# Optimization experiments

Hardware: AMD Instinct MI355X
Metric: run time of the kernel (lower is better)

The kernel has to match this reference:

```python
import jax, jax.numpy as jnp
import numpy as np

B, A, N_OBS, HX, N_ACT = 8192, 32, 128, 64, 16

def setup_inputs() -> dict:
    key = jax.random.key(0)
    ks = jax.random.split(key, 12)
    s = lambda *shape: 0.05 * jax.random.normal(ks[setup_inputs.i], shape, dtype=jnp.float32)
    out = {}
    setup_inputs.i = 0
    def nxt(*shape):
        setup_inputs.i += 1
        return 0.05 * jax.random.normal(ks[setup_inputs.i], shape, dtype=jnp.float32)
    out['obs'] = jax.random.normal(ks[0], (B, A, N_OBS), dtype=jnp.float32)
    out['W1'] = nxt(A, N_OBS, 128); out['b1'] = nxt(A, 128)
    out['W2'] = nxt(A, 128, HX);   out['b2'] = nxt(A, HX)
    out['Wg'] = nxt(A, HX, 2);     out['bg'] = nxt(A, 2)
    out['Wc'] = nxt(A, 2 * HX, HX); out['bc'] = nxt(A, HX)
    out['Wd'] = nxt(A, HX, N_ACT); out['bd'] = nxt(A, N_ACT)
    out['comm_mask'] = jax.random.randint(jax.random.fold_in(key, 99), (A, A), 0, 2, dtype=jnp.int32)
    return out

def reference(obs, W1, b1, W2, b2, Wg, bg, Wc, bc, Wd, bd, comm_mask):
    # encode: per-agent 2-layer MLP, batched over agents via einsum
    x = jax.nn.relu(jnp.einsum('ban,anh->bah', obs, W1) + b1)      # [B,A,128]
    h = jax.nn.relu(jnp.einsum('bah,ahk->bak', x, W2) + b2)        # [B,A,HX]
    # gate: Linear->ReLU->Softmax (computed as in original; only used via the
    # host-side RNG in the torch code, externalized here as comm_mask)
    gates = jax.nn.softmax(jax.nn.relu(jnp.einsum('bak,akg->bag', h, Wg) + bg), axis=-1)
    # communication: for agent i, mean of hidden states of communicating j != i
    mask = comm_mask.astype(h.dtype) * (1.0 - jnp.eye(A, dtype=h.dtype))  # [A_i, A_j]
    total = jnp.einsum('ij,bjk->bik', mask, h)                      # [B,A,HX]
    count = mask.sum(axis=1)                                        # [A]
    comm = total / jnp.maximum(count, 1.0)[None, :, None]           # count==0 -> zeros
    comm_in = jnp.concatenate([h, comm], axis=-1)                   # [B,A,2*HX]
    h2 = jnp.tanh(jnp.einsum('bac,ack->bak', comm_in, Wc) + bc)     # [B,A,HX]
    q = jnp.einsum('bak,akn->ban', h2, Wd) + bd                     # [B,A,N_ACT]
    return q
```

## Files before the change

kernel.cpp:

```cpp
#include <hip/hip_runtime.h>


#define NB   8192
#define NA   32
#define NOBS 128
#define NH1  128
#define HXX  64
#define NACT 16

typedef _Float16 half8 __attribute__((ext_vector_type(8)));
typedef _Float16 half4 __attribute__((ext_vector_type(4)));
typedef float    floatx4 __attribute__((ext_vector_type(4)));

#define MFMA16(af, bf, c) __builtin_amdgcn_mfma_f32_16x16x32_f16((af), (bf), (c), 0, 0, 0)
#define H8(x) __builtin_bit_cast(half8, (x))

#define HWS_OFF 0
#define W1P_OFF (NB * NA * HXX)
#define W1P_CNT (NA * 8 * 4 * 512)
#define W2P_OFF (W1P_OFF + W1P_CNT)
#define W2P_CNT (NA * 4 * 4 * 512)
#define WCP_OFF (W2P_OFF + W2P_CNT)
#define WCP_CNT (NA * 4 * 4 * 512)
#define WDP_OFF (WCP_OFF + WCP_CNT)
#define WDP_CNT (NA * 1 * 2 * 512)
#define MN_OFF  (WDP_OFF + WDP_CNT)

#define HSTR 2056
#define DEC_LDS (16 * HSTR * 2)

#define ENC_TILES 16
#define ENC_WROWS 256
#define ENC_BROWS 1024
#define ENC_DEPTH 4
#define ENC_SLAB  (ENC_DEPTH * 8192)
#define ENC_W2LDS (4 * ENC_SLAB)
#define ENC_LDS   (ENC_W2LDS + 16384)

#define PK_FRAG_BLOCKS 528
#define PK_BLOCKS      (PK_FRAG_BLOCKS + 4)

using gas1p = const __attribute__((address_space(1))) void*;
using las3p = __attribute__((address_space(3))) void*;

__device__ __forceinline__ float fast_tanh(float x) {
    x = fminf(fmaxf(x, -10.f), 10.f);
    float e2 = __expf(2.f * x);
    return (e2 - 1.f) / (e2 + 1.f);
}

extern "C" __global__ __launch_bounds__(256)
void pack_kernel(const float* __restrict__ W1,
                 const float* __restrict__ W2,
                 const float* __restrict__ Wc,
                 const float* __restrict__ Wd,
                 const int*   __restrict__ cmask,
                 _Float16* __restrict__ ws)
{
    __shared__ float stg[4][512];
    const int bid = blockIdx.x, tid = threadIdx.x;

    if (bid >= PK_FRAG_BLOCKS) {
        int r = (bid - PK_FRAG_BLOCKS) * 256 + tid;
        if (r >= NA * NA) return;
        int i = r >> 5, j = r & 31;
        int c = 0;
        for (int jj = 0; jj < NA; ++jj) c += (jj != i && cmask[i * NA + jj]) ? 1 : 0;
        float v = 0.f;
        if (j != i && cmask[i * NA + j]) v = 1.0f / (float)(c > 1 ? c : 1);
        ((float*)(ws + MN_OFF))[r] = v;
        return;
    }

    const int w = tid >> 6, l = tid & 63;
    const int W = bid * 4 + w;

    const float* src; _Float16* dst; int K, N;
    int a, nt, s;
    if (W < 1024) {
        int q = W; a = q >> 5; nt = (q >> 2) & 7; s = q & 3;
        src = W1; N = 128; K = 128;
        dst = ws + W1P_OFF + ((a * 8 + nt) * 4 + s) * 512;
    } else if (W < 1536) {
        int q = W - 1024; a = q >> 4; nt = (q >> 2) & 3; s = q & 3;
        src = W2; N = 64; K = 128;
        dst = ws + W2P_OFF + ((a * 4 + nt) * 4 + s) * 512;
    } else if (W < 2048) {
        int q = W - 1536; a = q >> 4; nt = (q >> 2) & 3; s = q & 3;
        src = Wc; N = 64; K = 128;
        dst = ws + WCP_OFF + ((a * 4 + nt) * 4 + s) * 512;
    } else {
        int q = W - 2048; a = q >> 1; nt = 0; s = q & 1;
        src = Wd; N = 16; K = 64;
        dst = ws + WDP_OFF + (a * 2 + s) * 512;
    }

    const float* base = src + (size_t)a * K * N + (size_t)(s * 32) * N + nt * 16;
    float* S = stg[w];

    #pragma unroll
    for (int p = 0; p < 8; ++p) {
        int e = p * 64 + l, kk = e >> 4, nn = e & 15;
        S[kk * 16 + nn] = base[(size_t)kk * N + nn];
    }
    asm volatile("s_waitcnt lgkmcnt(0)" ::: "memory");
    __builtin_amdgcn_sched_barrier(0);

    half8 hv;
    #pragma unroll
    for (int j = 0; j < 8; ++j)
        hv[j] = (_Float16)S[((l >> 4) * 8 + j) * 16 + (l & 15)];
    *(half8*)&dst[l * 8] = hv;
}

__device__ __forceinline__ void enc_wait_vm(int t) {
    switch (t) {
    case 0:  asm volatile("s_waitcnt vmcnt(24)" ::: "memory"); break;
    case 1:  asm volatile("s_waitcnt vmcnt(26)" ::: "memory"); break;
    case 2:  asm volatile("s_waitcnt vmcnt(28)" ::: "memory"); break;
    case 13: asm volatile("s_waitcnt vmcnt(22)" ::: "memory"); break;
    case 14: asm volatile("s_waitcnt vmcnt(14)" ::: "memory"); break;
    case 15: asm volatile("s_waitcnt vmcnt(6)"  ::: "memory"); break;
    default: asm volatile("s_waitcnt vmcnt(30)" ::: "memory"); break;
    }
}

extern "C" __global__ __launch_bounds__(256, 1)
void enc_kernel(const float* __restrict__ obs,
                const float* __restrict__ b1,
                const float* __restrict__ b2,
                const _Float16* __restrict__ W1p,
                const _Float16* __restrict__ W2p,
                _Float16* __restrict__ hws)
{
    extern __shared__ char smem[];

    const int tid  = threadIdx.x;
    const int a    = blockIdx.y;
    const int w    = tid >> 6, l = tid & 63;
    const int lm   = l & 15, lq = l >> 4;
    const int hrow = l >> 5;
    const int cch  = l & 31;
    char* SB = smem + w * ENC_SLAB;
    _Float16* W2L = (_Float16*)(smem + ENC_W2LDS);

    {
        const uint4* s = (const uint4*)(W2p + (size_t)a * (4 * 4 * 512));
        uint4* d = (uint4*)W2L;
        #pragma unroll
        for (int q = 0; q < 4; ++q) d[tid + 256 * q] = s[tid + 256 * q];
    }

    const int rowb = blockIdx.x * ENC_BROWS + w * ENC_WROWS;
    const char* ob = (const char*)obs + (size_t)rowb * (NA * NOBS * 4) + (size_t)a * (NOBS * 4);

    floatx4 w1r[8][4];
    #pragma unroll
    for (int nt = 0; nt < 8; ++nt)
        #pragma unroll
        for (int s = 0; s < 4; ++s)
            w1r[nt][s] = *(const floatx4*)&W1p[(((a * 8 + nt) * 4 + s) * 512) + l * 8];
    float b1v[8], b2v[4];
    #pragma unroll
    for (int nt = 0; nt < 8; ++nt) b1v[nt] = b1[a * NH1 + nt * 16 + lm];
    #pragma unroll
    for (int nt = 0; nt < 4; ++nt) b2v[nt] = b2[a * HXX + nt * 16 + lm];

    #pragma unroll
    for (int nt = 0; nt < 8; ++nt)
        #pragma unroll
        for (int s = 0; s < 4; ++s) asm volatile("" :: "v"(w1r[nt][s]));
    #pragma unroll
    for (int nt = 0; nt < 8; ++nt) asm volatile("" :: "v"(b1v[nt]));
    #pragma unroll
    for (int nt = 0; nt < 4; ++nt) asm volatile("" :: "v"(b2v[nt]));

    int dmaoff[8];
    #pragma unroll
    for (int i = 0; i < 8; ++i) {
        const int r = 2 * i + hrow;
        dmaoff[i] = r * (NA * NOBS * 4) + ((cch ^ (r & 7)) << 4);
    }

    auto issue = [&](int t) {
        const char* bt = ob + (size_t)t * (16 * NA * NOBS * 4);
        char* dstb = SB + (t & 3) * 8192;
        #pragma unroll
        for (int i = 0; i < 8; ++i)
            __builtin_amdgcn_global_load_lds((gas1p)(bt + dmaoff[i]),
                                             (las3p)(dstb + i * 1024), 16, 0, 0);
    };

    __syncthreads();

    issue(0); issue(1); issue(2);

    for (int t = 0; t < ENC_TILES; ++t) {
        char* SBp = SB + (t & 3) * 8192;

        asm volatile("s_waitcnt lgkmcnt(0)" ::: "memory");
        if (t <= ENC_TILES - 4) issue(t + 3);
        enc_wait_vm(t);
        __builtin_amdgcn_sched_barrier(0);

        _Float16* X = (_Float16*)SBp;
        const int rx = lm & 7;

        floatx4 acc1[8];
        #pragma unroll
        for (int nt = 0; nt < 8; ++nt) acc1[nt] = (floatx4){0.f, 0.f, 0.f, 0.f};
        #pragma unroll
        for (int s = 0; s < 4; ++s) {
            const int c0 = s * 8 + lq * 2;
            floatx4 f0 = *(const floatx4*)(SBp + lm * 512 + (((c0    ) ^ rx) << 4));
            floatx4 f1 = *(const floatx4*)(SBp + lm * 512 + (((c0 + 1) ^ rx) << 4));
            half8 af;
            af[0] = (_Float16)f0[0]; af[1] = (_Float16)f0[1];
            af[2] = (_Float16)f0[2]; af[3] = (_Float16)f0[3];
            af[4] = (_Float16)f1[0]; af[5] = (_Float16)f1[1];
            af[6] = (_Float16)f1[2]; af[7] = (_Float16)f1[3];
            #pragma unroll
            for (int nt = 0; nt < 8; ++nt)
                acc1[nt] = MFMA16(af, H8(w1r[nt][s]), acc1[nt]);
        }
        #pragma unroll
        for (int nt = 0; nt < 8; ++nt)
            #pragma unroll
            for (int v = 0; v < 4; ++v) {
                float xv = fmaxf(acc1[nt][v] + b1v[nt], 0.f);
                X[(lq * 4 + v) * 136 + nt * 16 + lm] = (_Float16)xv;
            }

        floatx4 acc2[4];
        #pragma unroll
        for (int nt = 0; nt < 4; ++nt) acc2[nt] = (floatx4){0.f, 0.f, 0.f, 0.f};
        #pragma unroll
        for (int s = 0; s < 4; ++s) {
            half8 af2 = *(const half8*)&X[lm * 136 + s * 32 + lq * 8];
            #pragma unroll
            for (int nt = 0; nt < 4; ++nt) {
                half8 bf = *(const half8*)&W2L[(nt * 4 + s) * 512 + l * 8];
                acc2[nt] = MFMA16(af2, bf, acc2[nt]);
            }
        }
        #pragma unroll
        for (int nt = 0; nt < 4; ++nt)
            #pragma unroll
            for (int v = 0; v < 4; ++v) {
                float hv = fmaxf(acc2[nt][v] + b2v[nt], 0.f);
                X[(lq * 4 + v) * 136 + nt * 16 + lm] = (_Float16)hv;
            }

        {
            const int rr = l >> 2, cc = l & 3;
            _Float16* hb = hws + ((size_t)(rowb + t * 16 + rr) * NA + a) * HXX;
            #pragma unroll
            for (int q2 = 0; q2 < 2; ++q2) {
                const int chunk = cc + 4 * q2;
                half8 hv8 = *(const half8*)&X[rr * 136 + chunk * 8];
                *(half8*)&hb[chunk * 8] = hv8;
            }
        }
    }
}

extern "C" __global__ __launch_bounds__(512)
void dec_kernel(const _Float16* __restrict__ hws,
                const float* __restrict__ MnG,
                const float* __restrict__ bc,
                const float* __restrict__ bd,
                const _Float16* __restrict__ Wcp,
                const _Float16* __restrict__ Wdp,
                float* __restrict__ out)
{
    extern __shared__ char smem[];
    _Float16* H = (_Float16*)smem;

    const int t  = threadIdx.x;
    const int b0 = blockIdx.x * 16;

    {
        const uint4* src = (const uint4*)(hws + (size_t)b0 * NA * HXX);
        #pragma unroll
        for (int it = 0; it < 8; ++it) {
            int idx = it * 512 + t;
            int row = idx >> 8, rem = idx & 255;
            *(uint4*)&H[row * HSTR + rem * 8] = src[idx];
        }
    }
    __syncthreads();

    const int w = t >> 6, l = t & 63, lm = l & 15, lq = l >> 4;

    half8 hacc[4][2];
    #pragma unroll
    for (int g = 0; g < 4; ++g)
        #pragma unroll
        for (int sb = 0; sb < 2; ++sb)
            #pragma unroll
            for (int q = 0; q < 8; ++q) hacc[g][sb][q] = (_Float16)0.f;

    #pragma unroll 4
    for (int j = 0; j < NA; ++j) {
        half8 v0 = *(const half8*)&H[lm * HSTR + j * 64 + lq * 8];
        half8 v1 = *(const half8*)&H[lm * HSTR + j * 64 + 32 + lq * 8];
        #pragma unroll
        for (int g = 0; g < 4; ++g) {
            int ag = __builtin_amdgcn_readfirstlane(w * 4 + g);
            _Float16 mh = (_Float16)MnG[ag * NA + j];
            hacc[g][0] += v0 * mh;
            hacc[g][1] += v1 * mh;
        }
    }
    __syncthreads();

    half4 h2r[4][4];
    #pragma unroll
    for (int nt = 0; nt < 4; ++nt) {
        floatx4 acc[4];
        #pragma unroll
        for (int g = 0; g < 4; ++g) acc[g] = (floatx4){0.f, 0.f, 0.f, 0.f};
        #pragma unroll
        for (int s = 0; s < 4; ++s) {
            #pragma unroll
            for (int g = 0; g < 4; ++g) {
                int ag = w * 4 + g;
                half8 af = (s < 2)
                    ? *(const half8*)&H[lm * HSTR + ag * 64 + s * 32 + lq * 8]
                    : hacc[g][s - 2];
                half8 bf = *(const half8*)&Wcp[(((ag * 4 + nt) * 4 + s) * 512) + l * 8];
                acc[g] = MFMA16(af, bf, acc[g]);
            }
        }
        #pragma unroll
        for (int g = 0; g < 4; ++g) {
            int ag = w * 4 + g;
            float bcv = bc[ag * HXX + nt * 16 + lm];
            #pragma unroll
            for (int v = 0; v < 4; ++v)
                h2r[g][nt][v] = (_Float16)fast_tanh(acc[g][v] + bcv);
        }
    }

    #pragma unroll
    for (int g = 0; g < 4; ++g) {
        int ag = w * 4 + g;
        #pragma unroll
        for (int nt = 0; nt < 4; ++nt)
            #pragma unroll
            for (int v = 0; v < 4; ++v)
                H[(lq * 4 + v) * HSTR + ag * 64 + nt * 16 + lm] = h2r[g][nt][v];
    }

    floatx4 acc3[4];
    #pragma unroll
    for (int g = 0; g < 4; ++g) acc3[g] = (floatx4){0.f, 0.f, 0.f, 0.f};
    #pragma unroll
    for (int s = 0; s < 2; ++s) {
        #pragma unroll
        for (int g = 0; g < 4; ++g) {
            int ag = w * 4 + g;
            half8 af = *(const half8*)&H[lm * HSTR + ag * 64 + s * 32 + lq * 8];
            half8 bf = *(const half8*)&Wdp[((ag * 2 + s) * 512) + l * 8];
            acc3[g] = MFMA16(af, bf, acc3[g]);
        }
    }

    #pragma unroll
    for (int g = 0; g < 4; ++g) {
        int ag = w * 4 + g;
        float bdv = bd[ag * NACT + lm];
        #pragma unroll
        for (int v = 0; v < 4; ++v) {
            int row = lq * 4 + v;
            out[((size_t)(b0 + row) * NA + ag) * NACT + lm] = acc3[g][v] + bdv;
        }
    }
}

extern "C" void kernel_launch(void* const* d_in, const int* in_sizes, int n_in,
                              void* d_out, int out_size, void* d_ws, size_t ws_size,
                              hipStream_t stream)
{
    const float* obs = (const float*)d_in[0];
    const float* W1  = (const float*)d_in[1];
    const float* b1  = (const float*)d_in[2];
    const float* W2  = (const float*)d_in[3];
    const float* b2  = (const float*)d_in[4];
    const float* Wc  = (const float*)d_in[7];
    const float* bc  = (const float*)d_in[8];
    const float* Wd  = (const float*)d_in[9];
    const float* bd  = (const float*)d_in[10];
    const int*   cm  = (const int*)d_in[11];

    float*    outp = (float*)d_out;
    _Float16* ws   = (_Float16*)d_ws;

    _Float16* hws = ws + HWS_OFF;
    _Float16* W1p = ws + W1P_OFF;
    _Float16* W2p = ws + W2P_OFF;
    _Float16* Wcp = ws + WCP_OFF;
    _Float16* Wdp = ws + WDP_OFF;
    const float* MnG = (const float*)(ws + MN_OFF);

    hipLaunchKernelGGL(pack_kernel, dim3(PK_BLOCKS), dim3(256), 0, stream,
                       W1, W2, Wc, Wd, cm, ws);

    (void)hipFuncSetAttribute((const void*)enc_kernel,
                              hipFuncAttributeMaxDynamicSharedMemorySize, ENC_LDS);
    hipLaunchKernelGGL(enc_kernel, dim3(NB / ENC_BROWS, NA), dim3(256), ENC_LDS,
                       stream, obs, b1, b2, W1p, W2p, hws);

    (void)hipFuncSetAttribute((const void*)dec_kernel,
                              hipFuncAttributeMaxDynamicSharedMemorySize, DEC_LDS);
    hipLaunchKernelGGL(dec_kernel, dim3(NB / 16), dim3(512), DEC_LDS, stream,
                       hws, MnG, bc, bd, Wcp, Wdp, outp);
}
```

Baseline: 275.5 us.

## Fuse encoder MLP into decoder kernel, dropping the hidden-state workspace round trip

Merges the per-agent encoder (two MFMA layers) into the decoder kernel, so each 512-thread block encodes its 16 batch rows for all 32 agents and writes h directly into LDS. This removes the fp16 h write to and reread from global memory, plus one launch. In exchange, the obs loads are plain global loads with no DMA pipelining, and W1/W2 fragments are reread from global/L2 by every block, where before they were kept in registers across 16 tiles.

```diff
diff --git a/kernel.cpp b/kernel.cpp
--- a/kernel.cpp
+++ b/kernel.cpp
@@ -13,7 +13,6 @@
 typedef float    floatx4 __attribute__((ext_vector_type(4)));
 
 #define MFMA16(af, bf, c) __builtin_amdgcn_mfma_f32_16x16x32_f16((af), (bf), (c), 0, 0, 0)
-#define H8(x) __builtin_bit_cast(half8, (x))
 
 #define HWS_OFF 0
 #define W1P_OFF (NB * NA * HXX)
@@ -27,21 +26,11 @@
 #define MN_OFF  (WDP_OFF + WDP_CNT)
 
 #define HSTR 2056
-#define DEC_LDS (16 * HSTR * 2)
-
-#define ENC_TILES 16
-#define ENC_WROWS 256
-#define ENC_BROWS 1024
-#define ENC_DEPTH 4
-#define ENC_SLAB  (ENC_DEPTH * 8192)
-#define ENC_W2LDS (4 * ENC_SLAB)
-#define ENC_LDS   (ENC_W2LDS + 16384)
+#define FUS_SLAB 4352
+#define FUS_LDS  (16 * HSTR * 2 + 8 * FUS_SLAB)
 
 #define PK_FRAG_BLOCKS 528
 #define PK_BLOCKS      (PK_FRAG_BLOCKS + 4)
-
-using gas1p = const __attribute__((address_space(1))) void*;
-using las3p = __attribute__((address_space(3))) void*;
 
 __device__ __forceinline__ float fast_tanh(float x) {
     x = fminf(fmaxf(x, -10.f), 10.f);
@@ -113,184 +102,87 @@
     *(half8*)&dst[l * 8] = hv;
 }
 
-__device__ __forceinline__ void enc_wait_vm(int t) {
-    switch (t) {
-    case 0:  asm volatile("s_waitcnt vmcnt(24)" ::: "memory"); break;
-    case 1:  asm volatile("s_waitcnt vmcnt(26)" ::: "memory"); break;
-    case 2:  asm volatile("s_waitcnt vmcnt(28)" ::: "memory"); break;
-    case 13: asm volatile("s_waitcnt vmcnt(22)" ::: "memory"); break;
-    case 14: asm volatile("s_waitcnt vmcnt(14)" ::: "memory"); break;
-    case 15: asm volatile("s_waitcnt vmcnt(6)"  ::: "memory"); break;
-    default: asm volatile("s_waitcnt vmcnt(30)" ::: "memory"); break;
-    }
-}
-
-extern "C" __global__ __launch_bounds__(256, 1)
-void enc_kernel(const float* __restrict__ obs,
-                const float* __restrict__ b1,
-                const float* __restrict__ b2,
-                const _Float16* __restrict__ W1p,
-                const _Float16* __restrict__ W2p,
-                _Float16* __restrict__ hws)
-{
-    extern __shared__ char smem[];
-
-    const int tid  = threadIdx.x;
-    const int a    = blockIdx.y;
-    const int w    = tid >> 6, l = tid & 63;
-    const int lm   = l & 15, lq = l >> 4;
-    const int hrow = l >> 5;
-    const int cch  = l & 31;
-    char* SB = smem + w * ENC_SLAB;
-    _Float16* W2L = (_Float16*)(smem + ENC_W2LDS);
-
-    {
-        const uint4* s = (const uint4*)(W2p + (size_t)a * (4 * 4 * 512));
-        uint4* d = (uint4*)W2L;
-        #pragma unroll
-        for (int q = 0; q < 4; ++q) d[tid + 256 * q] = s[tid + 256 * q];
-    }
-
-    const int rowb = blockIdx.x * ENC_BROWS + w * ENC_WROWS;
-    const char* ob = (const char*)obs + (size_t)rowb * (NA * NOBS * 4) + (size_t)a * (NOBS * 4);
-
-    floatx4 w1r[8][4];
-    #pragma unroll
-    for (int nt = 0; nt < 8; ++nt)
-        #pragma unroll
-        for (int s = 0; s < 4; ++s)
-            w1r[nt][s] = *(const floatx4*)&W1p[(((a * 8 + nt) * 4 + s) * 512) + l * 8];
-    float b1v[8], b2v[4];
-    #pragma unroll
-    for (int nt = 0; nt < 8; ++nt) b1v[nt] = b1[a * NH1 + nt * 16 + lm];
-    #pragma unroll
-    for (int nt = 0; nt < 4; ++nt) b2v[nt] = b2[a * HXX + nt * 16 + lm];
-
-    #pragma unroll
-    for (int nt = 0; nt < 8; ++nt)
-        #pragma unroll
-        for (int s = 0; s < 4; ++s) asm volatile("" :: "v"(w1r[nt][s]));
-    #pragma unroll
-    for (int nt = 0; nt < 8; ++nt) asm volatile("" :: "v"(b1v[nt]));
-    #pragma unroll
-    for (int nt = 0; nt < 4; ++nt) asm volatile("" :: "v"(b2v[nt]));
-
-    int dmaoff[8];
-    #pragma unroll
-    for (int i = 0; i < 8; ++i) {
-        const int r = 2 * i + hrow;
-        dmaoff[i] = r * (NA * NOBS * 4) + ((cch ^ (r & 7)) << 4);
-    }
-
-    auto issue = [&](int t) {
-        const char* bt = ob + (size_t)t * (16 * NA * NOBS * 4);
-        char* dstb = SB + (t & 3) * 8192;
-        #pragma unroll
-        for (int i = 0; i < 8; ++i)
-            __builtin_amdgcn_global_load_lds((gas1p)(bt + dmaoff[i]),
-                                             (las3p)(dstb + i * 1024), 16, 0, 0);
-    };
-
-    __syncthreads();
-
-    issue(0); issue(1); issue(2);
-
-    for (int t = 0; t < ENC_TILES; ++t) {
-        char* SBp = SB + (t & 3) * 8192;
-
-        asm volatile("s_waitcnt lgkmcnt(0)" ::: "memory");
-        if (t <= ENC_TILES - 4) issue(t + 3);
-        enc_wait_vm(t);
-        __builtin_amdgcn_sched_barrier(0);
-
-        _Float16* X = (_Float16*)SBp;
-        const int rx = lm & 7;
-
-        floatx4 acc1[8];
-        #pragma unroll
-        for (int nt = 0; nt < 8; ++nt) acc1[nt] = (floatx4){0.f, 0.f, 0.f, 0.f};
-        #pragma unroll
-        for (int s = 0; s < 4; ++s) {
-            const int c0 = s * 8 + lq * 2;
-            floatx4 f0 = *(const floatx4*)(SBp + lm * 512 + (((c0    ) ^ rx) << 4));
-            floatx4 f1 = *(const floatx4*)(SBp + lm * 512 + (((c0 + 1) ^ rx) << 4));
-            half8 af;
-            af[0] = (_Float16)f0[0]; af[1] = (_Float16)f0[1];
-            af[2] = (_Float16)f0[2]; af[3] = (_Float16)f0[3];
-            af[4] = (_Float16)f1[0]; af[5] = (_Float16)f1[1];
-            af[6] = (_Float16)f1[2]; af[7] = (_Float16)f1[3];
-            #pragma unroll
-            for (int nt = 0; nt < 8; ++nt)
-                acc1[nt] = MFMA16(af, H8(w1r[nt][s]), acc1[nt]);
-        }
-        #pragma unroll
-        for (int nt = 0; nt < 8; ++nt)
-            #pragma unroll
-            for (int v = 0; v < 4; ++v) {
-                float xv = fmaxf(acc1[nt][v] + b1v[nt], 0.f);
-                X[(lq * 4 + v) * 136 + nt * 16 + lm] = (_Float16)xv;
-            }
-
-        floatx4 acc2[4];
-        #pragma unroll
-        for (int nt = 0; nt < 4; ++nt) acc2[nt] = (floatx4){0.f, 0.f, 0.f, 0.f};
-        #pragma unroll
-        for (int s = 0; s < 4; ++s) {
-            half8 af2 = *(const half8*)&X[lm * 136 + s * 32 + lq * 8];
-            #pragma unroll
-            for (int nt = 0; nt < 4; ++nt) {
-                half8 bf = *(const half8*)&W2L[(nt * 4 + s) * 512 + l * 8];
-                acc2[nt] = MFMA16(af2, bf, acc2[nt]);
-            }
-        }
-        #pragma unroll
-        for (int nt = 0; nt < 4; ++nt)
-            #pragma unroll
-            for (int v = 0; v < 4; ++v) {
-                float hv = fmaxf(acc2[nt][v] + b2v[nt], 0.f);
-                X[(lq * 4 + v) * 136 + nt * 16 + lm] = (_Float16)hv;
-            }
-
-        {
-            const int rr = l >> 2, cc = l & 3;
-            _Float16* hb = hws + ((size_t)(rowb + t * 16 + rr) * NA + a) * HXX;
-            #pragma unroll
-            for (int q2 = 0; q2 < 2; ++q2) {
-                const int chunk = cc + 4 * q2;
-                half8 hv8 = *(const half8*)&X[rr * 136 + chunk * 8];
-                *(half8*)&hb[chunk * 8] = hv8;
-            }
-        }
-    }
-}
-
-extern "C" __global__ __launch_bounds__(512)
-void dec_kernel(const _Float16* __restrict__ hws,
-                const float* __restrict__ MnG,
-                const float* __restrict__ bc,
-                const float* __restrict__ bd,
-                const _Float16* __restrict__ Wcp,
-                const _Float16* __restrict__ Wdp,
-                float* __restrict__ out)
+extern "C" __global__ __launch_bounds__(512, 2)
+void fused_kernel(const float* __restrict__ obs,
+                  const float* __restrict__ b1,
+                  const float* __restrict__ b2,
+                  const float* __restrict__ MnG,
+                  const float* __restrict__ bc,
+                  const float* __restrict__ bd,
+                  const _Float16* __restrict__ W1p,
+                  const _Float16* __restrict__ W2p,
+                  const _Float16* __restrict__ Wcp,
+                  const _Float16* __restrict__ Wdp,
+                  float* __restrict__ out)
 {
     extern __shared__ char smem[];
     _Float16* H = (_Float16*)smem;
-
     const int t  = threadIdx.x;
     const int b0 = blockIdx.x * 16;
-
-    {
-        const uint4* src = (const uint4*)(hws + (size_t)b0 * NA * HXX);
-        #pragma unroll
-        for (int it = 0; it < 8; ++it) {
-            int idx = it * 512 + t;
-            int row = idx >> 8, rem = idx & 255;
-            *(uint4*)&H[row * HSTR + rem * 8] = src[idx];
+    const int w = t >> 6, l = t & 63, lm = l & 15, lq = l >> 4;
+    _Float16* XS = (_Float16*)(smem + 16 * HSTR * 2 + w * FUS_SLAB);
+
+    #pragma unroll
+    for (int g = 0; g < 4; ++g) {
+        const int ag = w * 4 + g;
+        const float* ob = obs + (size_t)(b0 + lm) * (NA * NOBS) + ag * NOBS;
+        floatx4 a0[4], a1[4];
+        #pragma unroll
+        for (int s = 0; s < 4; ++s) {
+            a0[s] = *(const floatx4*)&ob[s * 32 + lq * 8];
+            a1[s] = *(const floatx4*)&ob[s * 32 + lq * 8 + 4];
+        }
+        half8 af[4];
+        #pragma unroll
+        for (int s = 0; s < 4; ++s) {
+            af[s][0] = (_Float16)a0[s][0]; af[s][1] = (_Float16)a0[s][1];
+            af[s][2] = (_Float16)a0[s][2]; af[s][3] = (_Float16)a0[s][3];
+            af[s][4] = (_Float16)a1[s][0]; af[s][5] = (_Float16)a1[s][1];
+            af[s][6] = (_Float16)a1[s][2]; af[s][7] = (_Float16)a1[s][3];
+        }
+
+        floatx4 acc1[8];
+        #pragma unroll
+        for (int nt = 0; nt < 8; ++nt) acc1[nt] = (floatx4){0.f, 0.f, 0.f, 0.f};
+        #pragma unroll
+        for (int s = 0; s < 4; ++s) {
+            #pragma unroll
+            for (int nt = 0; nt < 8; ++nt) {
+                half8 bf = *(const half8*)&W1p[(((ag * 8 + nt) * 4 + s) * 512) + l * 8];
+                acc1[nt] = MFMA16(af[s], bf, acc1[nt]);
+            }
+        }
+        #pragma unroll
+        for (int nt = 0; nt < 8; ++nt) {
+            float bv = b1[ag * NH1 + nt * 16 + lm];
+            #pragma unroll
+            for (int v = 0; v < 4; ++v)
+                XS[(lq * 4 + v) * 136 + nt * 16 + lm] =
+                    (_Float16)fmaxf(acc1[nt][v] + bv, 0.f);
+        }
+
+        floatx4 acc2[4];
+        #pragma unroll
+        for (int nt = 0; nt < 4; ++nt) acc2[nt] = (floatx4){0.f, 0.f, 0.f, 0.f};
+        #pragma unroll
+        for (int s = 0; s < 4; ++s) {
+            half8 af2 = *(const half8*)&XS[lm * 136 + s * 32 + lq * 8];
+            #pragma unroll
+            for (int nt = 0; nt < 4; ++nt) {
+                half8 bf = *(const half8*)&W2p[(((ag * 4 + nt) * 4 + s) * 512) + l * 8];
+                acc2[nt] = MFMA16(af2, bf, acc2[nt]);
+            }
+        }
+        #pragma unroll
+        for (int nt = 0; nt < 4; ++nt) {
+            float bv = b2[ag * HXX + nt * 16 + lm];
+            #pragma unroll
+            for (int v = 0; v < 4; ++v)
+                H[(lq * 4 + v) * HSTR + ag * 64 + nt * 16 + lm] =
+                    (_Float16)fmaxf(acc2[nt][v] + bv, 0.f);
         }
     }
     __syncthreads();
-
-    const int w = t >> 6, l = t & 63, lm = l & 15, lq = l >> 4;
 
     half8 hacc[4][2];
     #pragma unroll
@@ -396,7 +288,6 @@
     float*    outp = (float*)d_out;
     _Float16* ws   = (_Float16*)d_ws;
 
-    _Float16* hws = ws + HWS_OFF;
     _Float16* W1p = ws + W1P_OFF;
     _Float16* W2p = ws + W2P_OFF;
     _Float16* Wcp = ws + WCP_OFF;
@@ -406,13 +297,8 @@
     hipLaunchKernelGGL(pack_kernel, dim3(PK_BLOCKS), dim3(256), 0, stream,
                        W1, W2, Wc, Wd, cm, ws);
 
-    (void)hipFuncSetAttribute((const void*)enc_kernel,
-                              hipFuncAttributeMaxDynamicSharedMemorySize, ENC_LDS);
-    hipLaunchKernelGGL(enc_kernel, dim3(NB / ENC_BROWS, NA), dim3(256), ENC_LDS,
-                       stream, obs, b1, b2, W1p, W2p, hws);
-
-    (void)hipFuncSetAttribute((const void*)dec_kernel,
-                              hipFuncAttributeMaxDynamicSharedMemorySize, DEC_LDS);
-    hipLaunchKernelGGL(dec_kernel, dim3(NB / 16), dim3(512), DEC_LDS, stream,
-                       hws, MnG, bc, bd, Wcp, Wdp, outp);
+    (void)hipFuncSetAttribute((const void*)fused_kernel,
+                              hipFuncAttributeMaxDynamicSharedMemorySize, FUS_LDS);
+    hipLaunchKernelGGL(fused_kernel, dim3(NB / 16), dim3(512), FUS_LDS, stream,
+                       obs, b1, b2, MnG, bc, bd, W1p, W2p, Wcp, Wdp, outp);
 }
```

Result: slower. 290.4 us (+5.4%).
